# Kernel optimization log

Hardware: AMD Instinct MI355X
Metric: run time of the kernel (lower is better)

Reference implementation:

```python
import jax, jax.numpy as jnp
import numpy as np

INF = 1.0e9
# 8-connected neighborhood (Warcraft shortest-path convention)
DIRS = [(-1, -1), (-1, 0), (-1, 1), (0, -1), (0, 1), (1, -1), (1, 0), (1, 1)]


def _shifted(d_KGG, di, dj):
    # shifted[i, j] = d[i + di, j + dj], INF out of bounds (di, dj static ints)
    K, G, _ = d_KGG.shape
    p = jnp.pad(d_KGG, ((0, 0), (1, 1), (1, 1)), constant_values=INF)
    return p[:, 1 + di:1 + di + G, 1 + dj:1 + dj + G]


def compute_shortest_path(cost_KGG):
    """Vertex-cost shortest path from (0,0) to (G-1,G-1) on an 8-connected grid.
    Returns a 0/1 mask of cells on the optimal path. Bellman-Ford style DP:
    G*G relaxation sweeps guarantee convergence for positive costs."""
    K, G, _ = cost_KGG.shape
    dist0 = jnp.full((K, G, G), INF, dtype=cost_KGG.dtype).at[:, 0, 0].set(cost_KGG[:, 0, 0])

    def relax(_, dist):
        nbr = dist  # placeholder; fold min over 8 shifted copies
        nbr = _shifted(dist, *DIRS[0])
        for d in DIRS[1:]:
            nbr = jnp.minimum(nbr, _shifted(dist, *d))
        return jnp.minimum(dist, cost_KGG + nbr)

    dist = jax.lax.fori_loop(0, G * G, relax, dist0)

    # Backtrack from (G-1, G-1): predecessor = argmin dist over 8 neighbors.
    di = jnp.array([d[0] for d in DIRS])
    dj = jnp.array([d[1] for d in DIRS])
    ks = jnp.arange(K)

    def step(carry, _):
        mask, pi, pj = carry
        ci = pi[:, None] + di[None, :]   # [K, 8]
        cj = pj[:, None] + dj[None, :]
        valid = (ci >= 0) & (ci < G) & (cj >= 0) & (cj < G)
        cic = jnp.clip(ci, 0, G - 1)
        cjc = jnp.clip(cj, 0, G - 1)
        nd = jnp.where(valid, dist[ks[:, None], cic, cjc], INF)
        best = jnp.argmin(nd, axis=-1)  # [K]
        npi = jnp.take_along_axis(cic, best[:, None], 1)[:, 0]
        npj = jnp.take_along_axis(cjc, best[:, None], 1)[:, 0]
        done = (pi == 0) & (pj == 0)
        pi2 = jnp.where(done, pi, npi)
        pj2 = jnp.where(done, pj, npj)
        mask2 = mask.at[ks, pi2, pj2].set(1.0)
        return (mask2, pi2, pj2), None

    mask0 = jnp.zeros((K, G, G), jnp.float32).at[:, G - 1, G - 1].set(1.0)
    p0 = jnp.full((K,), G - 1, dtype=jnp.int32)
    (mask, _, _), _ = jax.lax.scan(step, (mask0, p0, p0), None, length=G * G)
    return mask


def setup_inputs() -> dict:
    key = jax.random.key(0)
    S, B, G, n_costs = 8, 1024, 12, 5
    w_SBW = jax.random.randint(jax.random.fold_in(key, 1), (S, B, G * G), 0, n_costs)
    costs_t = jnp.array([0.8, 1.2, 5.3, 7.7, 9.2], dtype=jnp.float32)
    return {"w_SBW": w_SBW, "costs_t": costs_t}


def reference(w_SBW, costs_t):
    S, B, W = w_SBW.shape
    G = int(np.sqrt(W))
    w_KGG = w_SBW.reshape(S * B, G, G)
    cost_KGG = costs_t[w_KGG]          # embedding-style gather of per-cell costs
    y_KGG = compute_shortest_path(cost_KGG)
    return y_KGG.reshape(S, B, W).astype(jnp.int32)  # .long() in the original
```

## Files before the change

kernel.cpp:

```cpp
#include <hip/hip_runtime.h>
#include <float.h>

#define GDIM 12
#define NC   144
#define FINF 1.0e9f

__device__ __constant__ int DI8[8] = {-1, -1, -1, 0, 0, 1, 1, 1};
__device__ __constant__ int DJ8[8] = {-1,  0,  1,-1, 1,-1, 0, 1};

__device__ inline float dpp_shr1(float x) {
    return __int_as_float(__builtin_amdgcn_update_dpp(
        __float_as_int(FINF), __float_as_int(x), 0x111, 0xf, 0xf, false));
}
__device__ inline float dpp_shl1(float x) {
    return __int_as_float(__builtin_amdgcn_update_dpp(
        __float_as_int(FINF), __float_as_int(x), 0x101, 0xf, 0xf, false));
}

#define ROWUPD(i) {                                                  \
    float dm1 = ((i) > 0)        ? d[(i)-1] : FINF;                  \
    float dp1 = ((i) < GDIM - 1) ? d[(i)+1] : FINF;                  \
    float V   = fminf(dm1, dp1);                                     \
    float cm3 = fminf(V, d[(i)]);                                    \
    float L   = dpp_shr1(cm3);                                       \
    float R   = dpp_shl1(cm3);                                       \
    float nbr = fminf(fminf(L, R), V);                               \
    float nd  = c[(i)] + nbr;                                        \
    if (nd < d[(i)]) { d[(i)] = nd; changed = true; } }

__global__ __launch_bounds__(64)
void path_kernel(const int* __restrict__ w,
                 const float* __restrict__ costs,
                 int* __restrict__ out) {
    const int l = threadIdx.x;
    const int g = l >> 4;
    const int j = l & 15;
    const int pbase = blockIdx.x * 4;

    __shared__ int   s_w[4 * NC];
    __shared__ float dl[4][NC];
    __shared__ int   ml[4 * NC];

    const int* wblk = w + (size_t)pbase * NC;
    #pragma unroll
    for (int t = 0; t < 9; ++t) { s_w[t * 64 + l] = wblk[t * 64 + l]; ml[t * 64 + l] = 0; }
    __syncthreads();

    const bool act = (j < GDIM);
    float c[GDIM], d[GDIM];
    #pragma unroll
    for (int i = 0; i < GDIM; ++i) {
        c[i] = act ? costs[s_w[g * NC + i * GDIM + j]] : FINF;
        d[i] = FINF;
    }
    if (j == 0) d[0] = c[0];

    for (int it = 0; it < 200; ++it) {
        bool changed = false;
        if ((it & 1) == 0) {
            #pragma unroll
            for (int i = 0; i < GDIM; ++i) ROWUPD(i)
        } else {
            #pragma unroll
            for (int ii = 0; ii < GDIM; ++ii) { const int i = GDIM - 1 - ii; ROWUPD(i) }
        }
        if (__ballot(changed) == 0ull) break;
    }

    if (act) {
        #pragma unroll
        for (int i = 0; i < GDIM; ++i) dl[g][i * GDIM + j] = d[i];
    }
    __syncthreads();

    {
        const bool lead = (j == 0);
        int pi = GDIM - 1, pj = GDIM - 1;
        if (lead) ml[g * NC + NC - 1] = 1;
        bool walking = lead;
        for (int s = 0; s < NC; ++s) {
            if (__ballot(walking) == 0ull) break;
            if (walking) {
                if (pi == 0 && pj == 0) walking = false;
                else {
                    float best = FLT_MAX; int bi = pi, bj = pj;
                    #pragma unroll
                    for (int dd = 0; dd < 8; ++dd) {
                        int ci = pi + DI8[dd], cj = pj + DJ8[dd];
                        bool valid = (ci >= 0) & (ci < GDIM) & (cj >= 0) & (cj < GDIM);
                        int cic = min(max(ci, 0), GDIM - 1);
                        int cjc = min(max(cj, 0), GDIM - 1);
                        float v = valid ? dl[g][cic * GDIM + cjc] : FINF;
                        if (v < best) { best = v; bi = cic; bj = cjc; }
                    }
                    pi = bi; pj = bj;
                    ml[g * NC + pi * GDIM + pj] = 1;
                }
            }
        }
    }
    __syncthreads();

    int* outblk = out + (size_t)pbase * NC;
    #pragma unroll
    for (int t = 0; t < 9; ++t) outblk[t * 64 + l] = ml[t * 64 + l];
}

extern "C" void kernel_launch(void* const* d_in, const int* in_sizes, int n_in,
                              void* d_out, int out_size, void* d_ws, size_t ws_size,
                              hipStream_t stream) {
    const int*   w     = (const int*)d_in[0];
    const float* costs = (const float*)d_in[1];
    int*         out   = (int*)d_out;
    const int K = in_sizes[0] / NC;
    path_kernel<<<dim3(K / 4), dim3(64), 0, stream>>>(w, costs, out);
}
```

Measured before the change: 25.28 us.

## Use red-black row sweeps, rotating DPP, branchless relax and padded backtrack grid

Rows are relaxed in two parity passes (even rows, then odd rows) instead of alternating forward and backward sweeps. Convergence is checked only on the second of each pair of sweeps. The row-shift DPP now uses row rotation, relying on the inactive lanes 12-15 holding INF, and the relax step uses fminf instead of a branch. Backtracking runs on a 14x14 INF-padded shared grid, so neighbour lookups need no bounds checks, and it uses a while loop on one lane. The parity ordering may need more sweeps to converge than the sequential Gauss-Seidel sweeps did, but each sweep has more independent rows and fewer branches.

```diff
diff --git a/kernel.cpp b/kernel.cpp
--- a/kernel.cpp
+++ b/kernel.cpp
@@ -5,28 +5,33 @@
 #define NC   144
 #define FINF 1.0e9f
 
-__device__ __constant__ int DI8[8] = {-1, -1, -1, 0, 0, 1, 1, 1};
-__device__ __constant__ int DJ8[8] = {-1,  0,  1,-1, 1,-1, 0, 1};
-
-__device__ inline float dpp_shr1(float x) {
+__device__ inline float rotA(float x) {
     return __int_as_float(__builtin_amdgcn_update_dpp(
-        __float_as_int(FINF), __float_as_int(x), 0x111, 0xf, 0xf, false));
+        __float_as_int(x), __float_as_int(x), 0x121, 0xf, 0xf, false));
 }
-__device__ inline float dpp_shl1(float x) {
+__device__ inline float rotB(float x) {
     return __int_as_float(__builtin_amdgcn_update_dpp(
-        __float_as_int(FINF), __float_as_int(x), 0x101, 0xf, 0xf, false));
+        __float_as_int(x), __float_as_int(x), 0x12F, 0xf, 0xf, false));
 }
 
-#define ROWUPD(i) {                                                  \
-    float dm1 = ((i) > 0)        ? d[(i)-1] : FINF;                  \
-    float dp1 = ((i) < GDIM - 1) ? d[(i)+1] : FINF;                  \
-    float V   = fminf(dm1, dp1);                                     \
-    float cm3 = fminf(V, d[(i)]);                                    \
-    float L   = dpp_shr1(cm3);                                       \
-    float R   = dpp_shl1(cm3);                                       \
-    float nbr = fminf(fminf(L, R), V);                               \
-    float nd  = c[(i)] + nbr;                                        \
-    if (nd < d[(i)]) { d[(i)] = nd; changed = true; } }
+#define ROWU(i, TRACK) {                                                   \
+    float dm1 = ((i) > 0)        ? d[(i)-1] : FINF;                        \
+    float dp1 = ((i) < GDIM - 1) ? d[(i)+1] : FINF;                       \
+    float V   = fminf(dm1, dp1);                                           \
+    float cm3 = fminf(V, d[(i)]);                                          \
+    float nbr = fminf(fminf(rotA(cm3), rotB(cm3)), V);                     \
+    float nd  = c[(i)] + nbr;                                              \
+    if (TRACK) changed = changed | (nd < d[(i)]);                          \
+    d[(i)] = fminf(d[(i)], nd); }
+
+#define RB_SWEEP(TRACK) {                                                  \
+    _Pragma("unroll")                                                      \
+    for (int i = 0; i < GDIM; i += 2) ROWU(i, TRACK)                       \
+    _Pragma("unroll")                                                      \
+    for (int i = 1; i < GDIM; i += 2) ROWU(i, TRACK)                       \
+}
+
+__device__ __constant__ int POFF[8] = {-15, -14, -13, -1, 1, 13, 14, 15};
 
 __global__ __launch_bounds__(64)
 void path_kernel(const int* __restrict__ w,
@@ -38,12 +43,17 @@
     const int pbase = blockIdx.x * 4;
 
     __shared__ int   s_w[4 * NC];
-    __shared__ float dl[4][NC];
+    __shared__ float dl[4][196];
     __shared__ int   ml[4 * NC];
 
     const int* wblk = w + (size_t)pbase * NC;
     #pragma unroll
     for (int t = 0; t < 9; ++t) { s_w[t * 64 + l] = wblk[t * 64 + l]; ml[t * 64 + l] = 0; }
+    {
+        float* dlf = &dl[0][0];
+        #pragma unroll
+        for (int t = 0; t < 13; ++t) { int idx = t * 64 + l; if (idx < 784) dlf[idx] = FINF; }
+    }
     __syncthreads();
 
     const bool act = (j < GDIM);
@@ -55,48 +65,35 @@
     }
     if (j == 0) d[0] = c[0];
 
-    for (int it = 0; it < 200; ++it) {
+    for (int pair = 0; pair < 80; ++pair) {
         bool changed = false;
-        if ((it & 1) == 0) {
-            #pragma unroll
-            for (int i = 0; i < GDIM; ++i) ROWUPD(i)
-        } else {
-            #pragma unroll
-            for (int ii = 0; ii < GDIM; ++ii) { const int i = GDIM - 1 - ii; ROWUPD(i) }
-        }
+        RB_SWEEP(false)
+        RB_SWEEP(true)
         if (__ballot(changed) == 0ull) break;
     }
 
     if (act) {
         #pragma unroll
-        for (int i = 0; i < GDIM; ++i) dl[g][i * GDIM + j] = d[i];
+        for (int i = 0; i < GDIM; ++i) dl[g][(i + 1) * 14 + (j + 1)] = d[i];
     }
     __syncthreads();
 
-    {
-        const bool lead = (j == 0);
-        int pi = GDIM - 1, pj = GDIM - 1;
-        if (lead) ml[g * NC + NC - 1] = 1;
-        bool walking = lead;
-        for (int s = 0; s < NC; ++s) {
-            if (__ballot(walking) == 0ull) break;
-            if (walking) {
-                if (pi == 0 && pj == 0) walking = false;
-                else {
-                    float best = FLT_MAX; int bi = pi, bj = pj;
-                    #pragma unroll
-                    for (int dd = 0; dd < 8; ++dd) {
-                        int ci = pi + DI8[dd], cj = pj + DJ8[dd];
-                        bool valid = (ci >= 0) & (ci < GDIM) & (cj >= 0) & (cj < GDIM);
-                        int cic = min(max(ci, 0), GDIM - 1);
-                        int cjc = min(max(cj, 0), GDIM - 1);
-                        float v = valid ? dl[g][cic * GDIM + cjc] : FINF;
-                        if (v < best) { best = v; bi = cic; bj = cjc; }
-                    }
-                    pi = bi; pj = bj;
-                    ml[g * NC + pi * GDIM + pj] = 1;
-                }
+    if (j == 0) {
+        int a = 12 * 14 + 12;
+        ml[g * NC + NC - 1] = 1;
+        int guard = 0;
+        while (a != (1 * 14 + 1) && guard < 200) {
+            ++guard;
+            float best = FLT_MAX; int ba = a;
+            #pragma unroll
+            for (int dd = 0; dd < 8; ++dd) {
+                int na = a + POFF[dd];
+                float v = dl[g][na];
+                if (v < best) { best = v; ba = na; }
             }
+            a = ba;
+            int ii = a / 14 - 1, jj = a % 14 - 1;
+            ml[g * NC + ii * GDIM + jj] = 1;
         }
     }
     __syncthreads();
```

Result: faster. 24.43 us (-3.4%).
